# Optimization experiments

Hardware: AMD Instinct MI355X
Metric: run time of the kernel (lower is better)

The kernel has to match this reference:

```python
import jax, jax.numpy as jnp
import numpy as np

N, D, V = 262144, 3, 64
CAPACITY = 1 << 20  # hash table size (number of lattice vertices storable)
PRIMES = np.array([2654435761, 805459861, 3674653429], dtype=np.uint32)


def setup_inputs() -> dict:
    key = jax.random.key(0)
    k1, k2 = jax.random.split(key)
    positions = jax.random.normal(k1, (N, D), dtype=jnp.float32) * 2.0
    values = jax.random.normal(k2, (N, V), dtype=jnp.float32)
    return {"positions": positions, "values": values}


def _splat(positions, values):
    """Permutohedral-lattice splat: scatter-add barycentric-weighted homogeneous
    values into a hashed lattice table of shape [CAPACITY, V+1]."""
    n, d = positions.shape
    dp1 = d + 1
    # elevation scale factors (standard permutohedral construction)
    inv_std = np.sqrt(2.0 / 3.0) * dp1
    scale = (inv_std / np.sqrt((np.arange(d) + 1.0) * (np.arange(d) + 2.0))).astype(np.float32)
    cf = positions * scale                                   # [N, d]
    # elevated[i] = sum_{j>=i} cf_j - i * cf_{i-1}
    suf = jnp.cumsum(cf[:, ::-1], axis=1)[:, ::-1]           # suffix sums [N, d]
    suf_ext = jnp.concatenate([suf, jnp.zeros((n, 1), cf.dtype)], axis=1)  # [N, d+1]
    cf_pad = jnp.concatenate([jnp.zeros((n, 1), cf.dtype), cf], axis=1)
    i_arr = jnp.arange(dp1, dtype=cf.dtype)
    elev = suf_ext - i_arr * cf_pad                           # [N, d+1]

    # nearest 0-colored remainder point
    rd = jnp.round(elev / dp1)
    rem0 = rd * dp1                                           # [N, d+1]
    rd_sum = jnp.sum(rd, axis=1).astype(jnp.int32)            # [N]

    # rank: sort order of (elev - rem0), ties broken by index
    diff = elev - rem0
    dj = diff[:, :, None]
    di = diff[:, None, :]
    jidx = jnp.arange(dp1)[:, None]
    iidx = jnp.arange(dp1)[None, :]
    rank = jnp.sum(((dj > di) | ((dj == di) & (jidx < iidx))).astype(jnp.int32), axis=1)
    rank = rank + rd_sum[:, None]
    under = rank < 0
    over = rank > d
    rank = rank + jnp.where(under, dp1, 0) - jnp.where(over, dp1, 0)
    rem0 = rem0 + (under.astype(cf.dtype) - over.astype(cf.dtype)) * dp1

    # barycentric weights (length d+2, last entry folded into bary[0])
    delta = (elev - rem0) / dp1                               # [N, d+1]
    oh = (jax.nn.one_hot(d - rank, d + 2, dtype=cf.dtype)
          - jax.nn.one_hot(d + 1 - rank, d + 2, dtype=cf.dtype))  # [N, d+1, d+2]
    bary = jnp.einsum('nik,ni->nk', oh, delta)
    bary = bary.at[:, 0].add(1.0 + bary[:, d + 1])
    w = bary[:, :dp1]                                         # [N, d+1] simplex weights

    # simplex vertex keys per remainder r (only first d coords needed)
    r_arr = jnp.arange(dp1, dtype=jnp.int32)                  # [d+1]
    r_b = r_arr[None, :, None]                                # [1, d+1, 1]
    offs = jnp.where(rank[:, None, :d] < dp1 - r_b, r_b, r_b - dp1)  # [N, d+1, d]
    keys = rem0[:, None, :d].astype(jnp.int32) + offs         # [N, d+1, d]

    # hash keys into table slots
    h = (keys.astype(jnp.uint32) * jnp.asarray(PRIMES)).sum(-1) % jnp.uint32(CAPACITY)
    h = h.astype(jnp.int32)                                   # [N, d+1]

    # scatter-add weighted homogeneous values
    vh = jnp.concatenate([values, jnp.ones((n, 1), values.dtype)], axis=1)  # [N, V+1]
    contrib = w[:, :, None] * vh[:, None, :]                  # [N, d+1, V+1]
    table = jnp.zeros((CAPACITY, vh.shape[1]), values.dtype)
    table = table.at[h.reshape(-1)].add(contrib.reshape(-1, vh.shape[1]))
    return table


def reference(positions, values):
    return _splat(positions, values)
```

## Files before the change

### kernel.cpp

```cpp
#include <hip/hip_runtime.h>
#include <stdint.h>


#define CAPACITY (1u << 20)
#define KCAP     (1u << 20)
#define TBL_W    65
#define CHUNK    32

__device__ __forceinline__ void lattice_all(const float* __restrict__ pos, int point,
                                            uint32_t h[4], float w[4], uint32_t* keyOut)
{
    const float scale0 = 2.3094010767585034f;
    const float scale1 = 1.3333333333333333f;
    const float scale2 = 0.9428090415820634f;

    const float cf0 = pos[point * 3 + 0] * scale0;
    const float cf1 = pos[point * 3 + 1] * scale1;
    const float cf2 = pos[point * 3 + 2] * scale2;

    const float t1 = cf2 + cf1;
    float elev[4];
    elev[0] = t1 + cf0;
    elev[1] = t1 - cf0;
    elev[2] = cf2 - 2.0f * cf1;
    elev[3] = -3.0f * cf2;

    float rem0[4];
    float rd_s = 0.0f;
#pragma unroll
    for (int j = 0; j < 4; ++j) {
        float rd = rintf(elev[j] * 0.25f);
        rem0[j] = rd * 4.0f;
        rd_s += rd;
    }
    const int rd_sum = (int)rd_s;

    float diff[4];
#pragma unroll
    for (int j = 0; j < 4; ++j) diff[j] = elev[j] - rem0[j];

    int rank[4];
#pragma unroll
    for (int i = 0; i < 4; ++i) {
        int r = 0;
#pragma unroll
        for (int j = 0; j < 4; ++j) {
            if (diff[j] > diff[i] || (diff[j] == diff[i] && j < i)) r++;
        }
        rank[i] = r + rd_sum;
    }

#pragma unroll
    for (int i = 0; i < 4; ++i) {
        if (rank[i] < 0)      { rank[i] += 4; rem0[i] += 4.0f; }
        else if (rank[i] > 3) { rank[i] -= 4; rem0[i] -= 4.0f; }
    }

    float delta[4];
#pragma unroll
    for (int i = 0; i < 4; ++i) delta[i] = (elev[i] - rem0[i]) * 0.25f;

    float b[5] = {0.f, 0.f, 0.f, 0.f, 0.f};
#pragma unroll
    for (int i = 0; i < 4; ++i) {
        int k1 = 3 - rank[i];
        int k2 = 4 - rank[i];
        if (k1 >= 0 && k1 < 5) b[k1] += delta[i];
        if (k2 >= 0 && k2 < 5) b[k2] -= delta[i];
    }
    w[0] = b[0] + (1.0f + b[4]);
    w[1] = b[1];
    w[2] = b[2];
    w[3] = b[3];

    const uint32_t P0 = 2654435761u, P1 = 805459861u, P2 = 3674653429u;
    const int k0  = (int)rem0[0];
    const int k1i = (int)rem0[1];
    const int k2i = (int)rem0[2];

#pragma unroll
    for (int r = 0; r < 4; ++r) {
        int o0 = (rank[0] < 4 - r) ? r : r - 4;
        int o1 = (rank[1] < 4 - r) ? r : r - 4;
        int o2 = (rank[2] < 4 - r) ? r : r - 4;
        uint32_t hh = (uint32_t)(k0 + o0)  * P0
                    + (uint32_t)(k1i + o1) * P1
                    + (uint32_t)(k2i + o2) * P2;
        h[r] = hh & (CAPACITY - 1u);
    }

    const uint32_t pidx = (uint32_t)(rank[0] * 16 + rank[1] * 4 + rank[2]);
    uint32_t key = (uint32_t)k0 * P0 + (uint32_t)k1i * P1 + (uint32_t)k2i * P2
                 + pidx * 0x9E3779B9u;
    *keyOut = key & (KCAP - 1u);
}

__global__ __launch_bounds__(256) void k_hist(const float* __restrict__ pos,
                                              uint32_t* __restrict__ counts,
                                              uint32_t* __restrict__ keys, int n)
{
    int p = blockIdx.x * blockDim.x + threadIdx.x;
    if (p >= n) return;
    uint32_t h[4]; float w[4]; uint32_t key;
    lattice_all(pos, p, h, w, &key);
    keys[p] = key;
    atomicAdd(&counts[key], 1u);
}

__global__ __launch_bounds__(256) void k_blocksum(const uint32_t* __restrict__ counts,
                                                  uint32_t* __restrict__ partials)
{
    __shared__ uint32_t s[256];
    const int b = blockIdx.x, t = threadIdx.x;
    uint4 v = ((const uint4*)(counts + (size_t)b * 1024))[t];
    s[t] = v.x + v.y + v.z + v.w;
    __syncthreads();
    for (int o = 128; o > 0; o >>= 1) {
        if (t < o) s[t] += s[t + o];
        __syncthreads();
    }
    if (t == 0) partials[b] = s[0];
}

__global__ __launch_bounds__(1024) void k_scanpartials(uint32_t* __restrict__ partials)
{
    __shared__ uint32_t s[1024];
    const int t = threadIdx.x;
    const uint32_t v = partials[t];
    s[t] = v;
    __syncthreads();
    for (int o = 1; o < 1024; o <<= 1) {
        uint32_t x = s[t];
        uint32_t y = (t >= o) ? s[t - o] : 0u;
        __syncthreads();
        s[t] = x + y;
        __syncthreads();
    }
    partials[t] = s[t] - v;
}

__global__ __launch_bounds__(256) void k_offsets(const uint32_t* __restrict__ counts,
                                                 const uint32_t* __restrict__ partials,
                                                 uint32_t* __restrict__ offsets)
{
    __shared__ uint32_t s[256];
    const int b = blockIdx.x, t = threadIdx.x;
    uint4 v = ((const uint4*)(counts + (size_t)b * 1024))[t];
    const uint32_t s4 = v.x + v.y + v.z + v.w;
    s[t] = s4;
    __syncthreads();
    for (int o = 1; o < 256; o <<= 1) {
        uint32_t x = s[t];
        uint32_t y = (t >= o) ? s[t - o] : 0u;
        __syncthreads();
        s[t] = x + y;
        __syncthreads();
    }
    uint32_t texcl = (s[t] - s4) + partials[b];
    uint4 o4;
    o4.x = texcl;
    o4.y = texcl + v.x;
    o4.z = o4.y + v.y;
    o4.w = o4.z + v.z;
    ((uint4*)(offsets + (size_t)b * 1024))[t] = o4;
}

__global__ __launch_bounds__(256) void k_scatter(const uint32_t* __restrict__ keys,
                                                 const uint32_t* __restrict__ offsets,
                                                 uint32_t* __restrict__ counts,
                                                 uint32_t* __restrict__ sorted, int n)
{
    int p = blockIdx.x * blockDim.x + threadIdx.x;
    if (p >= n) return;
    const uint32_t key = keys[p];
    uint32_t slot = atomicSub(&counts[key], 1u) - 1u;
    sorted[offsets[key] + slot] = (uint32_t)p;
}

__global__ __launch_bounds__(256) void k_reduce(const uint32_t* __restrict__ sorted,
                                                const float* __restrict__ pos,
                                                const float* __restrict__ vals,
                                                float* __restrict__ table, int N)
{
    const int gtid = blockIdx.x * blockDim.x + threadIdx.x;
    const int wid  = gtid >> 6;
    const int lane = threadIdx.x & 63;
    const int base = wid * CHUNK;
    if (base >= N) return;
    const int cnt = min(CHUNK, N - base);

    const int e = (lane < cnt) ? lane : 0;
    const int mypid = (int)sorted[base + e];

    uint32_t mh[4]; float mw[4]; uint32_t dummyKey;
    lattice_all(pos, mypid, mh, mw, &dummyKey);

    uint32_t h0p = __shfl(mh[0], 0);
    uint32_t h1p = __shfl(mh[1], 0);
    uint32_t h2p = __shfl(mh[2], 0);
    uint32_t h3p = __shfl(mh[3], 0);

    float acc0 = 0.f, acc1 = 0.f, acc2 = 0.f, acc3 = 0.f;
    float aW0 = 0.f, aW1 = 0.f, aW2 = 0.f, aW3 = 0.f;

    for (int eb = 0; eb < cnt; eb += 8) {
        const int m = min(8, cnt - eb);
        float row[8];
#pragma unroll
        for (int j = 0; j < 8; ++j) {
            const int pj = __shfl(mypid, (eb + j) & (CHUNK - 1));
            row[j] = (j < m) ? vals[(size_t)pj * 64 + lane] : 0.f;
        }
#pragma unroll
        for (int j = 0; j < 8; ++j) {
            if (j >= m) break;
            const int src = eb + j;
            const uint32_t h0c = __shfl(mh[0], src);
            const uint32_t h1c = __shfl(mh[1], src);
            const uint32_t h2c = __shfl(mh[2], src);
            const uint32_t h3c = __shfl(mh[3], src);
            if ((h0c != h0p) | (h1c != h1p) | (h2c != h2p) | (h3c != h3p)) {
                atomicAdd(&table[(size_t)h0p * TBL_W + lane], acc0);
                atomicAdd(&table[(size_t)h1p * TBL_W + lane], acc1);
                atomicAdd(&table[(size_t)h2p * TBL_W + lane], acc2);
                atomicAdd(&table[(size_t)h3p * TBL_W + lane], acc3);
                if (lane == 0) {
                    atomicAdd(&table[(size_t)h0p * TBL_W + 64], aW0);
                    atomicAdd(&table[(size_t)h1p * TBL_W + 64], aW1);
                    atomicAdd(&table[(size_t)h2p * TBL_W + 64], aW2);
                    atomicAdd(&table[(size_t)h3p * TBL_W + 64], aW3);
                }
                acc0 = acc1 = acc2 = acc3 = 0.f;
                aW0 = aW1 = aW2 = aW3 = 0.f;
                h0p = h0c; h1p = h1c; h2p = h2c; h3p = h3c;
            }
            const float w0 = __shfl(mw[0], src);
            const float w1 = __shfl(mw[1], src);
            const float w2 = __shfl(mw[2], src);
            const float w3 = __shfl(mw[3], src);
            acc0 += w0 * row[j];
            acc1 += w1 * row[j];
            acc2 += w2 * row[j];
            acc3 += w3 * row[j];
            aW0 += w0; aW1 += w1; aW2 += w2; aW3 += w3;
        }
    }
    atomicAdd(&table[(size_t)h0p * TBL_W + lane], acc0);
    atomicAdd(&table[(size_t)h1p * TBL_W + lane], acc1);
    atomicAdd(&table[(size_t)h2p * TBL_W + lane], acc2);
    atomicAdd(&table[(size_t)h3p * TBL_W + lane], acc3);
    if (lane == 0) {
        atomicAdd(&table[(size_t)h0p * TBL_W + 64], aW0);
        atomicAdd(&table[(size_t)h1p * TBL_W + 64], aW1);
        atomicAdd(&table[(size_t)h2p * TBL_W + 64], aW2);
        atomicAdd(&table[(size_t)h3p * TBL_W + 64], aW3);
    }
}

__global__ __launch_bounds__(256) void splat_fallback(const float* __restrict__ pos,
                                                      const float* __restrict__ vals,
                                                      float* __restrict__ table, int n)
{
    const int gtid  = blockIdx.x * blockDim.x + threadIdx.x;
    const int point = gtid >> 6;
    const int lane  = threadIdx.x & 63;
    if (point >= n) return;
    uint32_t h[4]; float w[4]; uint32_t key;
    lattice_all(pos, point, h, w, &key);
    const float v = vals[(size_t)point * 64 + lane];
#pragma unroll
    for (int r = 0; r < 4; ++r)
        atomicAdd(&table[(size_t)h[r] * TBL_W + lane], w[r] * v);
    if (lane == 0) {
#pragma unroll
        for (int r = 0; r < 4; ++r)
            atomicAdd(&table[(size_t)h[r] * TBL_W + 64], w[r]);
    }
}

extern "C" void kernel_launch(void* const* d_in, const int* in_sizes, int n_in,
                              void* d_out, int out_size, void* d_ws, size_t ws_size,
                              hipStream_t stream) {
    const float* pos  = (const float*)d_in[0];
    const float* vals = (const float*)d_in[1];
    float* table      = (float*)d_out;

    const int n = in_sizes[0] / 3;

    hipMemsetAsync(d_out, 0, (size_t)out_size * sizeof(float), stream);

    const size_t SZ_CNT  = (size_t)KCAP * 4;
    const size_t offCnt  = 0;
    const size_t offOff  = offCnt + SZ_CNT;
    const size_t offPart = offOff + SZ_CNT;
    const size_t offKeys = offPart + 8192;
    const size_t offSort = offKeys + (size_t)n * 4;
    const size_t REQUIRED = offSort + (size_t)n * 4;

    if (ws_size < REQUIRED) {
        const int blocks = (n * 64 + 255) / 256;
        splat_fallback<<<blocks, 256, 0, stream>>>(pos, vals, table, n);
        return;
    }

    uint8_t* ws = (uint8_t*)d_ws;
    uint32_t* counts   = (uint32_t*)(ws + offCnt);
    uint32_t* offsets  = (uint32_t*)(ws + offOff);
    uint32_t* partials = (uint32_t*)(ws + offPart);
    uint32_t* keys     = (uint32_t*)(ws + offKeys);
    uint32_t* sorted   = (uint32_t*)(ws + offSort);

    hipMemsetAsync(counts, 0, SZ_CNT, stream);

    const int ptBlocks = (n + 255) / 256;
    k_hist<<<ptBlocks, 256, 0, stream>>>(pos, counts, keys, n);

    const int scanBlocks = KCAP / 1024;
    k_blocksum    <<<scanBlocks, 256,  0, stream>>>(counts, partials);
    k_scanpartials<<<1,          1024, 0, stream>>>(partials);
    k_offsets     <<<scanBlocks, 256,  0, stream>>>(counts, partials, offsets);

    k_scatter<<<ptBlocks, 256, 0, stream>>>(keys, offsets, counts, sorted, n);

    const int nWaves  = (n + CHUNK - 1) / CHUNK;
    const int rBlocks = (nWaves + 3) / 4;
    k_reduce<<<rBlocks, 256, 0, stream>>>(sorted, pos, vals, table, n);
}
```

Before: 135.3 us.

## Scan only occupied cells via compact cell list and record per-point slots

The histogram kernel now records each point's slot from the atomicAdd return value and appends each newly occupied key to a compact cell list. A single-block kernel then scans counts only over the occupied cells, replacing the three-kernel scan over the full 1M-entry count array. The scatter kernel no longer needs an atomicSub per point. The reduce chunk grows from 32 to 64 points per wave. The scan now runs in one 1024-thread block that loops over all occupied cells serially, which may be slow if there are many occupied cells. The cell order is arbitrary, which still groups points correctly.

```diff
diff --git a/kernel.cpp b/kernel.cpp
--- a/kernel.cpp
+++ b/kernel.cpp
@@ -5,7 +5,7 @@
 #define CAPACITY (1u << 20)
 #define KCAP     (1u << 20)
 #define TBL_W    65
-#define CHUNK    32
+#define CHUNK    64
 
 __device__ __forceinline__ void lattice_all(const float* __restrict__ pos, int point,
                                             uint32_t h[4], float w[4], uint32_t* keyOut)
@@ -97,84 +97,63 @@
 
 __global__ __launch_bounds__(256) void k_hist(const float* __restrict__ pos,
                                               uint32_t* __restrict__ counts,
-                                              uint32_t* __restrict__ keys, int n)
+                                              uint32_t* __restrict__ cursor,
+                                              uint32_t* __restrict__ cellList,
+                                              uint32_t* __restrict__ keys,
+                                              uint32_t* __restrict__ slots, int n)
 {
     int p = blockIdx.x * blockDim.x + threadIdx.x;
     if (p >= n) return;
     uint32_t h[4]; float w[4]; uint32_t key;
     lattice_all(pos, p, h, w, &key);
     keys[p] = key;
-    atomicAdd(&counts[key], 1u);
-}
-
-__global__ __launch_bounds__(256) void k_blocksum(const uint32_t* __restrict__ counts,
-                                                  uint32_t* __restrict__ partials)
-{
-    __shared__ uint32_t s[256];
-    const int b = blockIdx.x, t = threadIdx.x;
-    uint4 v = ((const uint4*)(counts + (size_t)b * 1024))[t];
-    s[t] = v.x + v.y + v.z + v.w;
-    __syncthreads();
-    for (int o = 128; o > 0; o >>= 1) {
-        if (t < o) s[t] += s[t + o];
-        __syncthreads();
-    }
-    if (t == 0) partials[b] = s[0];
-}
-
-__global__ __launch_bounds__(1024) void k_scanpartials(uint32_t* __restrict__ partials)
+    const uint32_t old = atomicAdd(&counts[key], 1u);
+    slots[p] = old;
+    if (old == 0u) {
+        const uint32_t idx = atomicAdd(cursor, 1u);
+        cellList[idx] = key;
+    }
+}
+
+__global__ __launch_bounds__(1024) void k_cscan(const uint32_t* __restrict__ counts,
+                                                const uint32_t* __restrict__ cellList,
+                                                const uint32_t* __restrict__ cursor,
+                                                uint32_t* __restrict__ offsets)
 {
     __shared__ uint32_t s[1024];
     const int t = threadIdx.x;
-    const uint32_t v = partials[t];
-    s[t] = v;
-    __syncthreads();
-    for (int o = 1; o < 1024; o <<= 1) {
-        uint32_t x = s[t];
-        uint32_t y = (t >= o) ? s[t - o] : 0u;
+    const uint32_t ncells = *cursor;
+    uint32_t carry = 0;
+
+    for (uint32_t base = 0; base < ncells; base += 1024u) {
+        const uint32_t i = base + (uint32_t)t;
+        uint32_t key = 0u, c = 0u;
+        if (i < ncells) { key = cellList[i]; c = counts[key]; }
+        s[t] = c;
         __syncthreads();
-        s[t] = x + y;
+        for (int o = 1; o < 1024; o <<= 1) {
+            uint32_t x = s[t];
+            uint32_t y = (t >= o) ? s[t - o] : 0u;
+            __syncthreads();
+            s[t] = x + y;
+            __syncthreads();
+        }
+        const uint32_t incl = s[t];
+        const uint32_t btot = s[1023];
+        if (i < ncells) offsets[key] = carry + incl - c;
+        carry += btot;
         __syncthreads();
     }
-    partials[t] = s[t] - v;
-}
-
-__global__ __launch_bounds__(256) void k_offsets(const uint32_t* __restrict__ counts,
-                                                 const uint32_t* __restrict__ partials,
-                                                 uint32_t* __restrict__ offsets)
-{
-    __shared__ uint32_t s[256];
-    const int b = blockIdx.x, t = threadIdx.x;
-    uint4 v = ((const uint4*)(counts + (size_t)b * 1024))[t];
-    const uint32_t s4 = v.x + v.y + v.z + v.w;
-    s[t] = s4;
-    __syncthreads();
-    for (int o = 1; o < 256; o <<= 1) {
-        uint32_t x = s[t];
-        uint32_t y = (t >= o) ? s[t - o] : 0u;
-        __syncthreads();
-        s[t] = x + y;
-        __syncthreads();
-    }
-    uint32_t texcl = (s[t] - s4) + partials[b];
-    uint4 o4;
-    o4.x = texcl;
-    o4.y = texcl + v.x;
-    o4.z = o4.y + v.y;
-    o4.w = o4.z + v.z;
-    ((uint4*)(offsets + (size_t)b * 1024))[t] = o4;
 }
 
 __global__ __launch_bounds__(256) void k_scatter(const uint32_t* __restrict__ keys,
+                                                 const uint32_t* __restrict__ slots,
                                                  const uint32_t* __restrict__ offsets,
-                                                 uint32_t* __restrict__ counts,
                                                  uint32_t* __restrict__ sorted, int n)
 {
     int p = blockIdx.x * blockDim.x + threadIdx.x;
     if (p >= n) return;
-    const uint32_t key = keys[p];
-    uint32_t slot = atomicSub(&counts[key], 1u) - 1u;
-    sorted[offsets[key] + slot] = (uint32_t)p;
+    sorted[offsets[keys[p]] + slots[p]] = (uint32_t)p;
 }
 
 __global__ __launch_bounds__(256) void k_reduce(const uint32_t* __restrict__ sorted,
@@ -289,12 +268,13 @@
 
     hipMemsetAsync(d_out, 0, (size_t)out_size * sizeof(float), stream);
 
-    const size_t SZ_CNT  = (size_t)KCAP * 4;
     const size_t offCnt  = 0;
-    const size_t offOff  = offCnt + SZ_CNT;
-    const size_t offPart = offOff + SZ_CNT;
-    const size_t offKeys = offPart + 8192;
-    const size_t offSort = offKeys + (size_t)n * 4;
+    const size_t offCur  = offCnt + (size_t)KCAP * 4;
+    const size_t offOff  = offCur + 64;
+    const size_t offCell = offOff + (size_t)KCAP * 4;
+    const size_t offKeys = offCell + (size_t)n * 4;
+    const size_t offSlot = offKeys + (size_t)n * 4;
+    const size_t offSort = offSlot + (size_t)n * 4;
     const size_t REQUIRED = offSort + (size_t)n * 4;
 
     if (ws_size < REQUIRED) {
@@ -305,22 +285,21 @@
 
     uint8_t* ws = (uint8_t*)d_ws;
     uint32_t* counts   = (uint32_t*)(ws + offCnt);
+    uint32_t* cursor   = (uint32_t*)(ws + offCur);
     uint32_t* offsets  = (uint32_t*)(ws + offOff);
-    uint32_t* partials = (uint32_t*)(ws + offPart);
+    uint32_t* cellList = (uint32_t*)(ws + offCell);
     uint32_t* keys     = (uint32_t*)(ws + offKeys);
+    uint32_t* slots    = (uint32_t*)(ws + offSlot);
     uint32_t* sorted   = (uint32_t*)(ws + offSort);
 
-    hipMemsetAsync(counts, 0, SZ_CNT, stream);
+    hipMemsetAsync(counts, 0, (size_t)KCAP * 4 + 64, stream);
 
     const int ptBlocks = (n + 255) / 256;
-    k_hist<<<ptBlocks, 256, 0, stream>>>(pos, counts, keys, n);
-
-    const int scanBlocks = KCAP / 1024;
-    k_blocksum    <<<scanBlocks, 256,  0, stream>>>(counts, partials);
-    k_scanpartials<<<1,          1024, 0, stream>>>(partials);
-    k_offsets     <<<scanBlocks, 256,  0, stream>>>(counts, partials, offsets);
-
-    k_scatter<<<ptBlocks, 256, 0, stream>>>(keys, offsets, counts, sorted, n);
+    k_hist<<<ptBlocks, 256, 0, stream>>>(pos, counts, cursor, cellList, keys, slots, n);
+
+    k_cscan<<<1, 1024, 0, stream>>>(counts, cellList, cursor, offsets);
+
+    k_scatter<<<ptBlocks, 256, 0, stream>>>(keys, slots, offsets, sorted, n);
 
     const int nWaves  = (n + CHUNK - 1) / CHUNK;
     const int rBlocks = (nWaves + 3) / 4;
```

Result: slower. 171.8 us (+27.0%).

## Record slot at histogram time, fold partial scan into offsets, widen chunk

Applied to the files above, without the earlier changes.

The histogram atomic now returns the per-key slot and stores it, so the scatter kernel no longer needs an atomicSub on the counts array. The separate single-block scan of the partials is removed: each offsets block sums all earlier partials itself, which drops one kernel launch at the cost of redundant reads. The reduce chunk grows from 32 to 64 points per wavefront, which lets the lane that handles each point cover a full 64-wide wave. This costs an extra per-point slot buffer in the workspace.

```diff
diff --git a/kernel.cpp b/kernel.cpp
--- a/kernel.cpp
+++ b/kernel.cpp
@@ -5,7 +5,7 @@
 #define CAPACITY (1u << 20)
 #define KCAP     (1u << 20)
 #define TBL_W    65
-#define CHUNK    32
+#define CHUNK    64
 
 __device__ __forceinline__ void lattice_all(const float* __restrict__ pos, int point,
                                             uint32_t h[4], float w[4], uint32_t* keyOut)
@@ -97,14 +97,15 @@
 
 __global__ __launch_bounds__(256) void k_hist(const float* __restrict__ pos,
                                               uint32_t* __restrict__ counts,
-                                              uint32_t* __restrict__ keys, int n)
+                                              uint32_t* __restrict__ keys,
+                                              uint32_t* __restrict__ slots, int n)
 {
     int p = blockIdx.x * blockDim.x + threadIdx.x;
     if (p >= n) return;
     uint32_t h[4]; float w[4]; uint32_t key;
     lattice_all(pos, p, h, w, &key);
     keys[p] = key;
-    atomicAdd(&counts[key], 1u);
+    slots[p] = atomicAdd(&counts[key], 1u);
 }
 
 __global__ __launch_bounds__(256) void k_blocksum(const uint32_t* __restrict__ counts,
@@ -122,29 +123,26 @@
     if (t == 0) partials[b] = s[0];
 }
 
-__global__ __launch_bounds__(1024) void k_scanpartials(uint32_t* __restrict__ partials)
-{
-    __shared__ uint32_t s[1024];
-    const int t = threadIdx.x;
-    const uint32_t v = partials[t];
-    s[t] = v;
-    __syncthreads();
-    for (int o = 1; o < 1024; o <<= 1) {
-        uint32_t x = s[t];
-        uint32_t y = (t >= o) ? s[t - o] : 0u;
-        __syncthreads();
-        s[t] = x + y;
-        __syncthreads();
-    }
-    partials[t] = s[t] - v;
-}
-
 __global__ __launch_bounds__(256) void k_offsets(const uint32_t* __restrict__ counts,
                                                  const uint32_t* __restrict__ partials,
-                                                 uint32_t* __restrict__ offsets)
+                                                 uint32_t* __restrict__ offsets,
+                                                 int nblocks)
 {
     __shared__ uint32_t s[256];
     const int b = blockIdx.x, t = threadIdx.x;
+
+    uint32_t mysum = 0;
+    for (int k = t; k < nblocks; k += 256)
+        if (k < b) mysum += partials[k];
+    s[t] = mysum;
+    __syncthreads();
+    for (int o = 128; o > 0; o >>= 1) {
+        if (t < o) s[t] += s[t + o];
+        __syncthreads();
+    }
+    const uint32_t base = s[0];
+    __syncthreads();
+
     uint4 v = ((const uint4*)(counts + (size_t)b * 1024))[t];
     const uint32_t s4 = v.x + v.y + v.z + v.w;
     s[t] = s4;
@@ -156,7 +154,7 @@
         s[t] = x + y;
         __syncthreads();
     }
-    uint32_t texcl = (s[t] - s4) + partials[b];
+    uint32_t texcl = (s[t] - s4) + base;
     uint4 o4;
     o4.x = texcl;
     o4.y = texcl + v.x;
@@ -166,15 +164,13 @@
 }
 
 __global__ __launch_bounds__(256) void k_scatter(const uint32_t* __restrict__ keys,
+                                                 const uint32_t* __restrict__ slots,
                                                  const uint32_t* __restrict__ offsets,
-                                                 uint32_t* __restrict__ counts,
                                                  uint32_t* __restrict__ sorted, int n)
 {
     int p = blockIdx.x * blockDim.x + threadIdx.x;
     if (p >= n) return;
-    const uint32_t key = keys[p];
-    uint32_t slot = atomicSub(&counts[key], 1u) - 1u;
-    sorted[offsets[key] + slot] = (uint32_t)p;
+    sorted[offsets[keys[p]] + slots[p]] = (uint32_t)p;
 }
 
 __global__ __launch_bounds__(256) void k_reduce(const uint32_t* __restrict__ sorted,
@@ -289,12 +285,12 @@
 
     hipMemsetAsync(d_out, 0, (size_t)out_size * sizeof(float), stream);
 
-    const size_t SZ_CNT  = (size_t)KCAP * 4;
     const size_t offCnt  = 0;
-    const size_t offOff  = offCnt + SZ_CNT;
-    const size_t offPart = offOff + SZ_CNT;
+    const size_t offOff  = offCnt + (size_t)KCAP * 4;
+    const size_t offPart = offOff + (size_t)KCAP * 4;
     const size_t offKeys = offPart + 8192;
-    const size_t offSort = offKeys + (size_t)n * 4;
+    const size_t offSlot = offKeys + (size_t)n * 4;
+    const size_t offSort = offSlot + (size_t)n * 4;
     const size_t REQUIRED = offSort + (size_t)n * 4;
 
     if (ws_size < REQUIRED) {
@@ -308,19 +304,19 @@
     uint32_t* offsets  = (uint32_t*)(ws + offOff);
     uint32_t* partials = (uint32_t*)(ws + offPart);
     uint32_t* keys     = (uint32_t*)(ws + offKeys);
+    uint32_t* slots    = (uint32_t*)(ws + offSlot);
     uint32_t* sorted   = (uint32_t*)(ws + offSort);
 
-    hipMemsetAsync(counts, 0, SZ_CNT, stream);
+    hipMemsetAsync(counts, 0, (size_t)KCAP * 4, stream);
 
     const int ptBlocks = (n + 255) / 256;
-    k_hist<<<ptBlocks, 256, 0, stream>>>(pos, counts, keys, n);
+    k_hist<<<ptBlocks, 256, 0, stream>>>(pos, counts, keys, slots, n);
 
     const int scanBlocks = KCAP / 1024;
-    k_blocksum    <<<scanBlocks, 256,  0, stream>>>(counts, partials);
-    k_scanpartials<<<1,          1024, 0, stream>>>(partials);
-    k_offsets     <<<scanBlocks, 256,  0, stream>>>(counts, partials, offsets);
-
-    k_scatter<<<ptBlocks, 256, 0, stream>>>(keys, offsets, counts, sorted, n);
+    k_blocksum<<<scanBlocks, 256, 0, stream>>>(counts, partials);
+    k_offsets <<<scanBlocks, 256, 0, stream>>>(counts, partials, offsets, scanBlocks);
+
+    k_scatter<<<ptBlocks, 256, 0, stream>>>(keys, slots, offsets, sorted, n);
 
     const int nWaves  = (n + CHUNK - 1) / CHUNK;
     const int rBlocks = (nWaves + 3) / 4;
```

New measurement: 113.5 us (median of 2 runs). 1.19x faster.
